# Optimization experiments

Hardware: AMD Instinct MI355X
Metric: run time of the kernel (lower is better)

The kernel has to match this reference:

```python
import jax, jax.numpy as jnp
import numpy as np

B, T, I, H, O = 1024, 512, 64, 256, 1

def setup_inputs() -> dict:
    key = jax.random.key(0)
    ks = jax.random.split(key, 12)
    s_ih0 = 1.0 / np.sqrt(H)
    def u(k, shape):
        return jax.random.uniform(k, shape, jnp.float32, -s_ih0, s_ih0)
    return {
        "x": jax.random.normal(ks[0], (B, T, I), jnp.float32),
        "w_ih0": u(ks[1], (4 * H, I)),
        "w_hh0": u(ks[2], (4 * H, H)),
        "b_ih0": u(ks[3], (4 * H,)),
        "b_hh0": u(ks[4], (4 * H,)),
        "w_ih1": u(ks[5], (4 * H, H)),
        "w_hh1": u(ks[6], (4 * H, H)),
        "b_ih1": u(ks[7], (4 * H,)),
        "b_hh1": u(ks[8], (4 * H,)),
        "fc_w": u(ks[9], (O, H)),
        "fc_b": u(ks[10], (O,)),
    }

def _lstm_layer(x, w_ih, w_hh, b_ih, b_hh):
    # x: [B, T, D_in] -> hidden sequence [B, T, H], gate order i,f,g,o (PyTorch)
    b, t, _ = x.shape
    h_dim = w_hh.shape[1]
    # precompute input projections for all timesteps: [T, B, 4H]
    xproj = (jnp.einsum('bti,gi->btg', x, w_ih) + b_ih + b_hh).transpose(1, 0, 2)
    h0 = jnp.zeros((b, h_dim), x.dtype)
    c0 = jnp.zeros((b, h_dim), x.dtype)

    def step(carry, xp):
        h, c = carry
        gates = xp + h @ w_hh.T  # [B, 4H]
        i_g, f_g, g_g, o_g = jnp.split(gates, 4, axis=-1)
        i_g = jax.nn.sigmoid(i_g)
        f_g = jax.nn.sigmoid(f_g)
        g_g = jnp.tanh(g_g)
        o_g = jax.nn.sigmoid(o_g)
        c = f_g * c + i_g * g_g
        h = o_g * jnp.tanh(c)
        return (h, c), h

    (h_last, _), hs = jax.lax.scan(step, (h0, c0), xproj)
    return hs.transpose(1, 0, 2), h_last

def reference(x, w_ih0, w_hh0, b_ih0, b_hh0, w_ih1, w_hh1, b_ih1, b_hh1, fc_w, fc_b):
    # Layer 0 -> (eval mode: dropout is identity) -> Layer 1 -> fc on last step
    h_seq0, _ = _lstm_layer(x, w_ih0, w_hh0, b_ih0, b_hh0)
    _, h_last1 = _lstm_layer(h_seq0, w_ih1, w_hh1, b_ih1, b_hh1)
    return h_last1 @ fc_w.T + fc_b  # [B, O]
```

## Files before the change

kernel.cpp:

```cpp
#include <hip/hip_runtime.h>
#include <stdint.h>


#define T_STEPS 512
#define NC0 10
#define NC1 16
#define WSLICE_ELEMS (4*(NC0+NC1)*512)
#define L1_OFF (4*NC0*512)
#define HN (1024*256)

typedef __attribute__((ext_vector_type(8))) short short8;
typedef __attribute__((ext_vector_type(4))) float floatx4;

__device__ __forceinline__ uint32_t f2bf(float f){
  uint32_t u = __builtin_bit_cast(uint32_t, f);
  return (u + 0x7fffu + ((u >> 16) & 1u)) >> 16;
}
__device__ __forceinline__ float bf2f(uint32_t b){
  return __builtin_bit_cast(float, b << 16);
}
__device__ __forceinline__ float sigm(float x){
  return __builtin_amdgcn_rcpf(1.0f + __builtin_amdgcn_exp2f(-1.44269504f*x));
}
__device__ __forceinline__ float tanhf_(float x){
  return 1.0f - 2.0f*__builtin_amdgcn_rcpf(1.0f + __builtin_amdgcn_exp2f(2.88539008f*x));
}
__device__ __forceinline__ floatx4 splat4(float v){ return (floatx4){v,v,v,v}; }

__device__ __forceinline__ short8 load_coh16(const uint16_t* p){
  short8 r;
  asm volatile("global_load_dwordx4 %0, %1, off sc0 sc1" : "=v"(r) : "v"(p));
  return r;
}
__device__ __forceinline__ void store_coh2(uint16_t* p, uint32_t v){
  asm volatile("global_store_short %0, %1, off sc0 sc1" :: "v"(p), "v"(v) : "memory");
}
__device__ __forceinline__ void vm_drain(){
  asm volatile("s_waitcnt vmcnt(0)" ::: "memory");
  __builtin_amdgcn_sched_barrier(0);
}

__device__ __forceinline__ void group_barrier(int* c, int target){
  vm_drain();
  __syncthreads();
  if (threadIdx.x == 0){
    __hip_atomic_fetch_add(c, 1, __ATOMIC_RELAXED, __HIP_MEMORY_SCOPE_AGENT);
    int spins = 0;
    while (__hip_atomic_load(c, __ATOMIC_RELAXED, __HIP_MEMORY_SCOPE_AGENT) < target){
      if (++spins > (1<<24)) break;
      __builtin_amdgcn_s_sleep(1);
    }
  }
  __syncthreads();
}

extern "C" __global__ void prep_weights(const float* __restrict__ wih0, const float* __restrict__ whh0,
                                        const float* __restrict__ wih1, const float* __restrict__ whh1,
                                        uint16_t* __restrict__ wfrag)
{
  int idx = blockIdx.x*256 + threadIdx.x;
  int s  = idx / WSLICE_ELEMS;
  int r  = idx - s*WSLICE_ELEMS;
  int layer = (r >= L1_OFF) ? 1 : 0;
  int rr = layer ? (r - L1_OFF) : r;
  int nc = layer ? NC1 : NC0;
  int n  = rr / (nc*512);
  int c  = (rr / 512) % nc;
  int l  = (rr >> 3) & 63;
  int j  = rr & 7;
  int k  = c*32 + ((l >> 4) << 3) + j;
  int grow = n*256 + s*16 + (l & 15);
  float v;
  if (!layer) v = (k < 64)  ? wih0[grow*64  + k] : whh0[grow*256 + (k - 64)];
  else        v = (k < 256) ? wih1[grow*256 + k] : whh1[grow*256 + (k - 256)];
  wfrag[idx] = (uint16_t)f2bf(v);
}

extern "C" __global__ void prep_bias(const float* __restrict__ bih0, const float* __restrict__ bhh0,
                                     const float* __restrict__ bih1, const float* __restrict__ bhh1,
                                     float* __restrict__ biasg)
{
  int idx = blockIdx.x*256 + threadIdx.x;
  if (idx >= 16*2*64) return;
  int s = idx >> 7;
  int layer = (idx >> 6) & 1;
  int q = idx & 63;
  int grow = (q >> 4)*256 + s*16 + (q & 15);
  biasg[idx] = layer ? (bih1[grow] + bhh1[grow]) : (bih0[grow] + bhh0[grow]);
}

extern "C" __global__ void __launch_bounds__(256, 1)
lstm_main(const float* __restrict__ x,
          const uint16_t* __restrict__ wfrag,
          const float* __restrict__ biasg,
          uint16_t* __restrict__ hbase,
          const float* __restrict__ fcw,
          const float* __restrict__ fcb,
          int* __restrict__ ctr,
          float* __restrict__ out)
{
  extern __shared__ uint16_t wlds[];
  const int tid  = threadIdx.x;
  const int bid  = blockIdx.x;
  const int s    = bid >> 4;
  const int g    = bid & 15;
  const int wv   = tid >> 6;
  const int lane = tid & 63;

  {
    const uint16_t* wsrc = wfrag + (size_t)s*WSLICE_ELEMS;
    for (int i = tid*8; i < WSLICE_ELEMS; i += 256*8)
      *(short8*)(wlds + i) = *(const short8*)(wsrc + i);
  }
  float b0[4], b1[4];
  {
    const int col = lane & 15;
    #pragma unroll
    for (int n = 0; n < 4; ++n){
      b0[n] = biasg[(s*2+0)*64 + n*16 + col];
      b1[n] = biasg[(s*2+1)*64 + n*16 + col];
    }
  }
  __syncthreads();

  const int arow = g*64 + wv*16 + (lane & 15);
  const int ka   = (lane >> 4) * 8;
  const int drow = g*64 + wv*16 + ((lane >> 4) << 2);
  const int dcol = s*16 + (lane & 15);

  uint16_t* h0hi[2] = { hbase + 0*(size_t)HN, hbase + 1*(size_t)HN };
  uint16_t* h0lo[2] = { hbase + 2*(size_t)HN, hbase + 3*(size_t)HN };
  uint16_t* h1hi[2] = { hbase + 4*(size_t)HN, hbase + 5*(size_t)HN };
  uint16_t* h1lo[2] = { hbase + 6*(size_t)HN, hbase + 7*(size_t)HN };

  float c0[4] = {0,0,0,0}, c1[4] = {0,0,0,0};
  int* myc = ctr + g*32;

  short8 ahi[NC0], alo[NC0];
  short8 bh[8],  bl[8];

  for (int t = 0; t < T_STEPS; ++t){
    const int par = t & 1, rpar = par ^ 1;

    {
      const float* xp = x + ((size_t)arow*T_STEPS + t)*64 + ka;
      #pragma unroll
      for (int kc = 0; kc < 2; ++kc){
        floatx4 v0 = *(const floatx4*)(xp + kc*32);
        floatx4 v1 = *(const floatx4*)(xp + kc*32 + 4);
        #pragma unroll
        for (int j = 0; j < 8; ++j){
          float f = (j < 4) ? v0[j] : v1[j-4];
          uint32_t hb = f2bf(f);
          float fh = bf2f(hb);
          uint32_t lb = f2bf(f - fh);
          ahi[kc][j] = (short)hb; alo[kc][j] = (short)lb;
        }
      }
    }
    {
      const uint16_t* ph  = h0hi[rpar] + (size_t)arow*256 + ka;
      const uint16_t* pl  = h0lo[rpar] + (size_t)arow*256 + ka;
      const uint16_t* p1h = h1hi[rpar] + (size_t)arow*256 + ka;
      const uint16_t* p1l = h1lo[rpar] + (size_t)arow*256 + ka;
      #pragma unroll
      for (int kc = 0; kc < 8; ++kc){
        ahi[2+kc] = load_coh16(ph  + kc*32);
        alo[2+kc] = load_coh16(pl  + kc*32);
        bh[kc]    = load_coh16(p1h + kc*32);
        bl[kc]    = load_coh16(p1l + kc*32);
      }
    }

    floatx4 acc[4];
    #pragma unroll
    for (int n = 0; n < 4; ++n) acc[n] = splat4(b0[n]);
    #pragma unroll
    for (int pk = 0; pk < 2; ++pk){
      #pragma unroll
      for (int n = 0; n < 4; ++n){
        short8 bfr = *(const short8*)(wlds + (n*NC0 + pk)*512 + lane*8);
        acc[n] = __builtin_amdgcn_mfma_f32_16x16x32_bf16(ahi[pk], bfr, acc[n], 0, 0, 0);
        acc[n] = __builtin_amdgcn_mfma_f32_16x16x32_bf16(alo[pk], bfr, acc[n], 0, 0, 0);
      }
    }
    vm_drain();
    #pragma unroll
    for (int pk = 2; pk < NC0; ++pk){
      #pragma unroll
      for (int n = 0; n < 4; ++n){
        short8 bfr = *(const short8*)(wlds + (n*NC0 + pk)*512 + lane*8);
        acc[n] = __builtin_amdgcn_mfma_f32_16x16x32_bf16(ahi[pk], bfr, acc[n], 0, 0, 0);
        acc[n] = __builtin_amdgcn_mfma_f32_16x16x32_bf16(alo[pk], bfr, acc[n], 0, 0, 0);
      }
    }
    {
      uint16_t* qh = h0hi[par]; uint16_t* ql = h0lo[par];
      #pragma unroll
      for (int r = 0; r < 4; ++r){
        float ig = sigm(acc[0][r]);
        float fg = sigm(acc[1][r]);
        float gg = tanhf_(acc[2][r]);
        float og = sigm(acc[3][r]);
        c0[r] = fg*c0[r] + ig*gg;
        float h = og*tanhf_(c0[r]);
        uint32_t hb = f2bf(h); float fh = bf2f(hb); uint32_t lb = f2bf(h - fh);
        size_t idx = (size_t)(drow + r)*256 + dcol;
        store_coh2(qh + idx, hb); store_coh2(ql + idx, lb);
      }
    }
    group_barrier(myc, 16*(2*t+1));

    {
      const uint16_t* p0h = h0hi[par] + (size_t)arow*256 + ka;
      const uint16_t* p0l = h0lo[par] + (size_t)arow*256 + ka;
      #pragma unroll
      for (int kc = 0; kc < 8; ++kc){
        ahi[kc] = load_coh16(p0h + kc*32);
        alo[kc] = load_coh16(p0l + kc*32);
      }
    }
    #pragma unroll
    for (int n = 0; n < 4; ++n) acc[n] = splat4(b1[n]);
    #pragma unroll
    for (int pk = 8; pk < NC1; ++pk){
      #pragma unroll
      for (int n = 0; n < 4; ++n){
        short8 bfr = *(const short8*)(wlds + L1_OFF + (n*NC1 + pk)*512 + lane*8);
        acc[n] = __builtin_amdgcn_mfma_f32_16x16x32_bf16(bh[pk-8], bfr, acc[n], 0, 0, 0);
        acc[n] = __builtin_amdgcn_mfma_f32_16x16x32_bf16(bl[pk-8], bfr, acc[n], 0, 0, 0);
      }
    }
    vm_drain();
    #pragma unroll
    for (int pk = 0; pk < 8; ++pk){
      #pragma unroll
      for (int n = 0; n < 4; ++n){
        short8 bfr = *(const short8*)(wlds + L1_OFF + (n*NC1 + pk)*512 + lane*8);
        acc[n] = __builtin_amdgcn_mfma_f32_16x16x32_bf16(ahi[pk], bfr, acc[n], 0, 0, 0);
        acc[n] = __builtin_amdgcn_mfma_f32_16x16x32_bf16(alo[pk], bfr, acc[n], 0, 0, 0);
      }
    }
    {
      uint16_t* qh = h1hi[par]; uint16_t* ql = h1lo[par];
      #pragma unroll
      for (int r = 0; r < 4; ++r){
        float ig = sigm(acc[0][r]);
        float fg = sigm(acc[1][r]);
        float gg = tanhf_(acc[2][r]);
        float og = sigm(acc[3][r]);
        c1[r] = fg*c1[r] + ig*gg;
        float h = og*tanhf_(c1[r]);
        uint32_t hb = f2bf(h); float fh = bf2f(hb); uint32_t lb = f2bf(h - fh);
        size_t idx = (size_t)(drow + r)*256 + dcol;
        store_coh2(qh + idx, hb); store_coh2(ql + idx, lb);
      }
    }
    group_barrier(myc, 16*(2*t+2));
  }

  if (s == 0){
    const uint16_t* fh = h1hi[1];
    const uint16_t* fl = h1lo[1];
    const int rl = tid >> 2, seg = tid & 3;
    const int row = g*64 + rl;
    short8 vh[8], vl[8];
    #pragma unroll
    for (int c = 0; c < 8; ++c){
      vh[c] = load_coh16(fh + (size_t)row*256 + seg*64 + c*8);
      vl[c] = load_coh16(fl + (size_t)row*256 + seg*64 + c*8);
    }
    vm_drain();
    float sum = 0.f;
    #pragma unroll
    for (int c = 0; c < 8; ++c){
      #pragma unroll
      for (int j = 0; j < 8; ++j){
        int k = seg*64 + c*8 + j;
        sum += (bf2f((uint16_t)vh[c][j]) + bf2f((uint16_t)vl[c][j])) * fcw[k];
      }
    }
    sum += __shfl_down(sum, 1);
    sum += __shfl_down(sum, 2);
    if (seg == 0) out[row] = sum + fcb[0];
  }
}

extern "C" void kernel_launch(void* const* d_in, const int* in_sizes, int n_in,
                              void* d_out, int out_size, void* d_ws, size_t ws_size,
                              hipStream_t stream)
{
  (void)in_sizes; (void)n_in; (void)out_size; (void)ws_size;
  const float* x    = (const float*)d_in[0];
  const float* wih0 = (const float*)d_in[1];
  const float* whh0 = (const float*)d_in[2];
  const float* bih0 = (const float*)d_in[3];
  const float* bhh0 = (const float*)d_in[4];
  const float* wih1 = (const float*)d_in[5];
  const float* whh1 = (const float*)d_in[6];
  const float* bih1 = (const float*)d_in[7];
  const float* bhh1 = (const float*)d_in[8];
  const float* fcw  = (const float*)d_in[9];
  const float* fcb  = (const float*)d_in[10];

  char* ws = (char*)d_ws;
  const size_t SZ_WFRAG = (size_t)16*WSLICE_ELEMS*2;
  const size_t OFF_BIAS = SZ_WFRAG;
  const size_t OFF_CTR  = OFF_BIAS + (size_t)16*2*64*4;
  const size_t OFF_H    = (size_t)2*1024*1024;

  uint16_t* wfrag = (uint16_t*)(ws);
  float*    biasg = (float*)(ws + OFF_BIAS);
  int*      ctr   = (int*)(ws + OFF_CTR);
  uint16_t* hbase = (uint16_t*)(ws + OFF_H);
  float*    out   = (float*)d_out;

  hipMemsetAsync(ws + OFF_CTR, 0, (OFF_H - OFF_CTR) + (size_t)8*HN*2, stream);

  hipLaunchKernelGGL(prep_weights, dim3(16*WSLICE_ELEMS/256), dim3(256), 0, stream,
                     wih0, whh0, wih1, whh1, wfrag);
  hipLaunchKernelGGL(prep_bias, dim3(8), dim3(256), 0, stream,
                     bih0, bhh0, bih1, bhh1, biasg);

  hipFuncSetAttribute((const void*)lstm_main,
                      hipFuncAttributeMaxDynamicSharedMemorySize, WSLICE_ELEMS*2);
  void* args[] = { (void*)&x, (void*)&wfrag, (void*)&biasg, (void*)&hbase,
                   (void*)&fcw, (void*)&fcb, (void*)&ctr, (void*)&out };
  hipLaunchCooperativeKernel((void*)lstm_main, dim3(256), dim3(256),
                             args, WSLICE_ELEMS*2, stream);
}
```

Measured before the change: 5.390 ms.

## Skew layer-1 one step behind layer-0 to halve per-step group barriers

Restructures the time loop so layer 1 processes step t-1 while layer 0 processes step t. The two layers then share one group barrier per iteration instead of two, and layer-1's input projection reuses the same loaded h0 fragments. Next-step x is prefetched and converted during compute, partial vmcnt waits replace full drains, and the final FC is fused into a last-step epilogue using shuffle reductions and atomicAdd into a zeroed output. This adds an epilogue step, a non-cooperative launch fallback, and relies on careful vmcnt counting for correctness.

```diff
diff --git a/kernel.cpp b/kernel.cpp
--- a/kernel.cpp
+++ b/kernel.cpp
@@ -27,32 +27,30 @@
 }
 __device__ __forceinline__ floatx4 splat4(float v){ return (floatx4){v,v,v,v}; }
 
+__device__ __forceinline__ void cvt8(const floatx4& v0, const floatx4& v1, short8& hi, short8& lo){
+  #pragma unroll
+  for (int j = 0; j < 8; ++j){
+    float f = (j < 4) ? v0[j] : v1[j-4];
+    uint32_t hb = f2bf(f); float fh = bf2f(hb); uint32_t lb = f2bf(f - fh);
+    hi[j] = (short)hb; lo[j] = (short)lb;
+  }
+}
+
 __device__ __forceinline__ short8 load_coh16(const uint16_t* p){
   short8 r;
   asm volatile("global_load_dwordx4 %0, %1, off sc0 sc1" : "=v"(r) : "v"(p));
   return r;
 }
+__device__ __forceinline__ floatx4 load_g16f(const float* p){
+  floatx4 r;
+  asm volatile("global_load_dwordx4 %0, %1, off" : "=v"(r) : "v"(p));
+  return r;
+}
 __device__ __forceinline__ void store_coh2(uint16_t* p, uint32_t v){
   asm volatile("global_store_short %0, %1, off sc0 sc1" :: "v"(p), "v"(v) : "memory");
 }
-__device__ __forceinline__ void vm_drain(){
-  asm volatile("s_waitcnt vmcnt(0)" ::: "memory");
-  __builtin_amdgcn_sched_barrier(0);
-}
-
-__device__ __forceinline__ void group_barrier(int* c, int target){
-  vm_drain();
-  __syncthreads();
-  if (threadIdx.x == 0){
-    __hip_atomic_fetch_add(c, 1, __ATOMIC_RELAXED, __HIP_MEMORY_SCOPE_AGENT);
-    int spins = 0;
-    while (__hip_atomic_load(c, __ATOMIC_RELAXED, __HIP_MEMORY_SCOPE_AGENT) < target){
-      if (++spins > (1<<24)) break;
-      __builtin_amdgcn_s_sleep(1);
-    }
-  }
-  __syncthreads();
-}
+#define VM_WAIT(N) do{ asm volatile("s_waitcnt vmcnt(" #N ")" ::: "memory"); \
+                       __builtin_amdgcn_sched_barrier(0); }while(0)
 
 extern "C" __global__ void prep_weights(const float* __restrict__ wih0, const float* __restrict__ whh0,
                                         const float* __restrict__ wih1, const float* __restrict__ whh1,
@@ -107,6 +105,11 @@
   const int wv   = tid >> 6;
   const int lane = tid & 63;
 
+  const int arow = g*64 + wv*16 + (lane & 15);
+  const int ka   = (lane >> 4) * 8;
+  const int drow = g*64 + wv*16 + ((lane >> 4) << 2);
+  const int dcol = s*16 + (lane & 15);
+
   {
     const uint16_t* wsrc = wfrag + (size_t)s*WSLICE_ELEMS;
     for (int i = tid*8; i < WSLICE_ELEMS; i += 256*8)
@@ -121,87 +124,93 @@
       b1[n] = biasg[(s*2+1)*64 + n*16 + col];
     }
   }
+  const float fcwv = fcw[dcol];
+  const float fcb0 = fcb[0];
+
+  short8 xh[2], xl[2];
+  {
+    const float* xp = x + (size_t)arow*T_STEPS*64 + ka;
+    floatx4 v0 = *(const floatx4*)(xp);
+    floatx4 v1 = *(const floatx4*)(xp + 4);
+    floatx4 v2 = *(const floatx4*)(xp + 32);
+    floatx4 v3 = *(const floatx4*)(xp + 36);
+    cvt8(v0, v1, xh[0], xl[0]);
+    cvt8(v2, v3, xh[1], xl[1]);
+  }
   __syncthreads();
 
-  const int arow = g*64 + wv*16 + (lane & 15);
-  const int ka   = (lane >> 4) * 8;
-  const int drow = g*64 + wv*16 + ((lane >> 4) << 2);
-  const int dcol = s*16 + (lane & 15);
-
-  uint16_t* h0hi[2] = { hbase + 0*(size_t)HN, hbase + 1*(size_t)HN };
-  uint16_t* h0lo[2] = { hbase + 2*(size_t)HN, hbase + 3*(size_t)HN };
-  uint16_t* h1hi[2] = { hbase + 4*(size_t)HN, hbase + 5*(size_t)HN };
-  uint16_t* h1lo[2] = { hbase + 6*(size_t)HN, hbase + 7*(size_t)HN };
-
+  const size_t abase = (size_t)arow*256 + ka;
   float c0[4] = {0,0,0,0}, c1[4] = {0,0,0,0};
   int* myc = ctr + g*32;
 
-  short8 ahi[NC0], alo[NC0];
-  short8 bh[8],  bl[8];
-
   for (int t = 0; t < T_STEPS; ++t){
-    const int par = t & 1, rpar = par ^ 1;
-
+    const size_t par0  = (size_t)(t & 1);
+    const size_t rpar0 = par0 ^ 1;
+
+    short8 a0h[8], a0l[8], a1h[8], a1l[8];
     {
-      const float* xp = x + ((size_t)arow*T_STEPS + t)*64 + ka;
-      #pragma unroll
-      for (int kc = 0; kc < 2; ++kc){
-        floatx4 v0 = *(const floatx4*)(xp + kc*32);
-        floatx4 v1 = *(const floatx4*)(xp + kc*32 + 4);
-        #pragma unroll
-        for (int j = 0; j < 8; ++j){
-          float f = (j < 4) ? v0[j] : v1[j-4];
-          uint32_t hb = f2bf(f);
-          float fh = bf2f(hb);
-          uint32_t lb = f2bf(f - fh);
-          ahi[kc][j] = (short)hb; alo[kc][j] = (short)lb;
-        }
-      }
+      const uint16_t* ph = hbase + rpar0*HN              + abase;
+      const uint16_t* pl = hbase + 2*(size_t)HN + rpar0*HN + abase;
+      #pragma unroll
+      for (int kc = 0; kc < 8; ++kc) a0h[kc] = load_coh16(ph + kc*32);
+      #pragma unroll
+      for (int kc = 0; kc < 8; ++kc) a0l[kc] = load_coh16(pl + kc*32);
     }
     {
-      const uint16_t* ph  = h0hi[rpar] + (size_t)arow*256 + ka;
-      const uint16_t* pl  = h0lo[rpar] + (size_t)arow*256 + ka;
-      const uint16_t* p1h = h1hi[rpar] + (size_t)arow*256 + ka;
-      const uint16_t* p1l = h1lo[rpar] + (size_t)arow*256 + ka;
-      #pragma unroll
-      for (int kc = 0; kc < 8; ++kc){
-        ahi[2+kc] = load_coh16(ph  + kc*32);
-        alo[2+kc] = load_coh16(pl  + kc*32);
-        bh[kc]    = load_coh16(p1h + kc*32);
-        bl[kc]    = load_coh16(p1l + kc*32);
-      }
-    }
-
-    floatx4 acc[4];
-    #pragma unroll
-    for (int n = 0; n < 4; ++n) acc[n] = splat4(b0[n]);
+      const uint16_t* ph = hbase + 4*(size_t)HN + par0*HN + abase;
+      const uint16_t* pl = hbase + 6*(size_t)HN + par0*HN + abase;
+      #pragma unroll
+      for (int kc = 0; kc < 8; ++kc) a1h[kc] = load_coh16(ph + kc*32);
+      #pragma unroll
+      for (int kc = 0; kc < 8; ++kc) a1l[kc] = load_coh16(pl + kc*32);
+    }
+    floatx4 xr0, xr1, xr2, xr3;
+    {
+      const int tn = (t < T_STEPS-1) ? (t+1) : t;
+      const float* xp = x + ((size_t)arow*T_STEPS + tn)*64 + ka;
+      xr0 = load_g16f(xp);      xr1 = load_g16f(xp + 4);
+      xr2 = load_g16f(xp + 32); xr3 = load_g16f(xp + 36);
+    }
+
+    floatx4 acc0[4], acc1[4];
+    #pragma unroll
+    for (int n = 0; n < 4; ++n) acc0[n] = splat4(b0[n]);
     #pragma unroll
     for (int pk = 0; pk < 2; ++pk){
       #pragma unroll
       for (int n = 0; n < 4; ++n){
-        short8 bfr = *(const short8*)(wlds + (n*NC0 + pk)*512 + lane*8);
-        acc[n] = __builtin_amdgcn_mfma_f32_16x16x32_bf16(ahi[pk], bfr, acc[n], 0, 0, 0);
-        acc[n] = __builtin_amdgcn_mfma_f32_16x16x32_bf16(alo[pk], bfr, acc[n], 0, 0, 0);
-      }
-    }
-    vm_drain();
-    #pragma unroll
-    for (int pk = 2; pk < NC0; ++pk){
+        short8 w = *(const short8*)(wlds + (n*NC0 + pk)*512 + lane*8);
+        acc0[n] = __builtin_amdgcn_mfma_f32_16x16x32_bf16(xh[pk], w, acc0[n], 0, 0, 0);
+        acc0[n] = __builtin_amdgcn_mfma_f32_16x16x32_bf16(xl[pk], w, acc0[n], 0, 0, 0);
+      }
+    }
+    #pragma unroll
+    for (int n = 0; n < 4; ++n) acc1[n] = splat4(b1[n]);
+
+    VM_WAIT(20);
+
+    #pragma unroll
+    for (int kc = 0; kc < 8; ++kc){
       #pragma unroll
       for (int n = 0; n < 4; ++n){
-        short8 bfr = *(const short8*)(wlds + (n*NC0 + pk)*512 + lane*8);
-        acc[n] = __builtin_amdgcn_mfma_f32_16x16x32_bf16(ahi[pk], bfr, acc[n], 0, 0, 0);
-        acc[n] = __builtin_amdgcn_mfma_f32_16x16x32_bf16(alo[pk], bfr, acc[n], 0, 0, 0);
-      }
-    }
+        short8 w0 = *(const short8*)(wlds + (n*NC0 + 2 + kc)*512 + lane*8);
+        acc0[n] = __builtin_amdgcn_mfma_f32_16x16x32_bf16(a0h[kc], w0, acc0[n], 0, 0, 0);
+        acc0[n] = __builtin_amdgcn_mfma_f32_16x16x32_bf16(a0l[kc], w0, acc0[n], 0, 0, 0);
+        short8 w1 = *(const short8*)(wlds + L1_OFF + (n*NC1 + kc)*512 + lane*8);
+        acc1[n] = __builtin_amdgcn_mfma_f32_16x16x32_bf16(a0h[kc], w1, acc1[n], 0, 0, 0);
+        acc1[n] = __builtin_amdgcn_mfma_f32_16x16x32_bf16(a0l[kc], w1, acc1[n], 0, 0, 0);
+      }
+    }
+
     {
-      uint16_t* qh = h0hi[par]; uint16_t* ql = h0lo[par];
+      uint16_t* qh = hbase + par0*HN;
+      uint16_t* ql = hbase + 2*(size_t)HN + par0*HN;
       #pragma unroll
       for (int r = 0; r < 4; ++r){
-        float ig = sigm(acc[0][r]);
-        float fg = sigm(acc[1][r]);
-        float gg = tanhf_(acc[2][r]);
-        float og = sigm(acc[3][r]);
+        float ig = sigm(acc0[0][r]);
+        float fg = sigm(acc0[1][r]);
+        float gg = tanhf_(acc0[2][r]);
+        float og = sigm(acc0[3][r]);
         c0[r] = fg*c0[r] + ig*gg;
         float h = og*tanhf_(c0[r]);
         uint32_t hb = f2bf(h); float fh = bf2f(hb); uint32_t lb = f2bf(h - fh);
@@ -209,46 +218,32 @@
         store_coh2(qh + idx, hb); store_coh2(ql + idx, lb);
       }
     }
-    group_barrier(myc, 16*(2*t+1));
-
-    {
-      const uint16_t* p0h = h0hi[par] + (size_t)arow*256 + ka;
-      const uint16_t* p0l = h0lo[par] + (size_t)arow*256 + ka;
-      #pragma unroll
-      for (int kc = 0; kc < 8; ++kc){
-        ahi[kc] = load_coh16(p0h + kc*32);
-        alo[kc] = load_coh16(p0l + kc*32);
-      }
-    }
-    #pragma unroll
-    for (int n = 0; n < 4; ++n) acc[n] = splat4(b1[n]);
-    #pragma unroll
-    for (int pk = 8; pk < NC1; ++pk){
+
+    VM_WAIT(12);
+
+    #pragma unroll
+    for (int kc = 0; kc < 8; ++kc){
       #pragma unroll
       for (int n = 0; n < 4; ++n){
-        short8 bfr = *(const short8*)(wlds + L1_OFF + (n*NC1 + pk)*512 + lane*8);
-        acc[n] = __builtin_amdgcn_mfma_f32_16x16x32_bf16(bh[pk-8], bfr, acc[n], 0, 0, 0);
-        acc[n] = __builtin_amdgcn_mfma_f32_16x16x32_bf16(bl[pk-8], bfr, acc[n], 0, 0, 0);
-      }
-    }
-    vm_drain();
-    #pragma unroll
-    for (int pk = 0; pk < 8; ++pk){
-      #pragma unroll
-      for (int n = 0; n < 4; ++n){
-        short8 bfr = *(const short8*)(wlds + L1_OFF + (n*NC1 + pk)*512 + lane*8);
-        acc[n] = __builtin_amdgcn_mfma_f32_16x16x32_bf16(ahi[pk], bfr, acc[n], 0, 0, 0);
-        acc[n] = __builtin_amdgcn_mfma_f32_16x16x32_bf16(alo[pk], bfr, acc[n], 0, 0, 0);
-      }
-    }
-    {
-      uint16_t* qh = h1hi[par]; uint16_t* ql = h1lo[par];
+        short8 w1 = *(const short8*)(wlds + L1_OFF + (n*NC1 + 8 + kc)*512 + lane*8);
+        acc1[n] = __builtin_amdgcn_mfma_f32_16x16x32_bf16(a1h[kc], w1, acc1[n], 0, 0, 0);
+        acc1[n] = __builtin_amdgcn_mfma_f32_16x16x32_bf16(a1l[kc], w1, acc1[n], 0, 0, 0);
+      }
+    }
+
+    VM_WAIT(8);
+    cvt8(xr0, xr1, xh[0], xl[0]);
+    cvt8(xr2, xr3, xh[1], xl[1]);
+
+    if (t > 0){
+      uint16_t* qh = hbase + 4*(size_t)HN + rpar0*HN;
+      uint16_t* ql = hbase + 6*(size_t)HN + rpar0*HN;
       #pragma unroll
       for (int r = 0; r < 4; ++r){
-        float ig = sigm(acc[0][r]);
-        float fg = sigm(acc[1][r]);
-        float gg = tanhf_(acc[2][r]);
-        float og = sigm(acc[3][r]);
+        float ig = sigm(acc1[0][r]);
+        float fg = sigm(acc1[1][r]);
+        float gg = tanhf_(acc1[2][r]);
+        float og = sigm(acc1[3][r]);
         c1[r] = fg*c1[r] + ig*gg;
         float h = og*tanhf_(c1[r]);
         uint32_t hb = f2bf(h); float fh = bf2f(hb); uint32_t lb = f2bf(h - fh);
@@ -256,33 +251,69 @@
         store_coh2(qh + idx, hb); store_coh2(ql + idx, lb);
       }
     }
-    group_barrier(myc, 16*(2*t+2));
-  }
-
-  if (s == 0){
-    const uint16_t* fh = h1hi[1];
-    const uint16_t* fl = h1lo[1];
-    const int rl = tid >> 2, seg = tid & 3;
-    const int row = g*64 + rl;
-    short8 vh[8], vl[8];
-    #pragma unroll
-    for (int c = 0; c < 8; ++c){
-      vh[c] = load_coh16(fh + (size_t)row*256 + seg*64 + c*8);
-      vl[c] = load_coh16(fl + (size_t)row*256 + seg*64 + c*8);
-    }
-    vm_drain();
-    float sum = 0.f;
-    #pragma unroll
-    for (int c = 0; c < 8; ++c){
-      #pragma unroll
-      for (int j = 0; j < 8; ++j){
-        int k = seg*64 + c*8 + j;
-        sum += (bf2f((uint16_t)vh[c][j]) + bf2f((uint16_t)vl[c][j])) * fcw[k];
-      }
-    }
-    sum += __shfl_down(sum, 1);
-    sum += __shfl_down(sum, 2);
-    if (seg == 0) out[row] = sum + fcb[0];
+
+    VM_WAIT(0);
+
+    __syncthreads();
+    if (tid == 0){
+      __hip_atomic_fetch_add(myc, 1, __ATOMIC_RELAXED, __HIP_MEMORY_SCOPE_AGENT);
+      const int target = 16*(t+1);
+      int spins = 0;
+      while (__hip_atomic_load(myc, __ATOMIC_RELAXED, __HIP_MEMORY_SCOPE_AGENT) < target){
+        if (++spins > (1<<20)) break;
+        __builtin_amdgcn_s_sleep(1);
+      }
+    }
+    __syncthreads();
+  }
+
+  {
+    const uint16_t* p0h = hbase + 1*(size_t)HN + abase;
+    const uint16_t* p0l = hbase + 3*(size_t)HN + abase;
+    const uint16_t* p1h = hbase + 4*(size_t)HN + abase;
+    const uint16_t* p1l = hbase + 6*(size_t)HN + abase;
+    short8 a0h[8], a0l[8], a1h[8], a1l[8];
+    #pragma unroll
+    for (int kc = 0; kc < 8; ++kc){
+      a0h[kc] = load_coh16(p0h + kc*32);
+      a0l[kc] = load_coh16(p0l + kc*32);
+      a1h[kc] = load_coh16(p1h + kc*32);
+      a1l[kc] = load_coh16(p1l + kc*32);
+    }
+    VM_WAIT(0);
+    floatx4 acc[4];
+    #pragma unroll
+    for (int n = 0; n < 4; ++n) acc[n] = splat4(b1[n]);
+    #pragma unroll
+    for (int kc = 0; kc < 8; ++kc){
+      #pragma unroll
+      for (int n = 0; n < 4; ++n){
+        short8 w1 = *(const short8*)(wlds + L1_OFF + (n*NC1 + kc)*512 + lane*8);
+        acc[n] = __builtin_amdgcn_mfma_f32_16x16x32_bf16(a0h[kc], w1, acc[n], 0, 0, 0);
+        acc[n] = __builtin_amdgcn_mfma_f32_16x16x32_bf16(a0l[kc], w1, acc[n], 0, 0, 0);
+        short8 w2 = *(const short8*)(wlds + L1_OFF + (n*NC1 + 8 + kc)*512 + lane*8);
+        acc[n] = __builtin_amdgcn_mfma_f32_16x16x32_bf16(a1h[kc], w2, acc[n], 0, 0, 0);
+        acc[n] = __builtin_amdgcn_mfma_f32_16x16x32_bf16(a1l[kc], w2, acc[n], 0, 0, 0);
+      }
+    }
+    #pragma unroll
+    for (int r = 0; r < 4; ++r){
+      float ig = sigm(acc[0][r]);
+      float fg = sigm(acc[1][r]);
+      float gg = tanhf_(acc[2][r]);
+      float og = sigm(acc[3][r]);
+      float cc = fg*c1[r] + ig*gg;
+      float h  = og*tanhf_(cc);
+      float v  = h * fcwv;
+      v += __shfl_xor(v, 1);
+      v += __shfl_xor(v, 2);
+      v += __shfl_xor(v, 4);
+      v += __shfl_xor(v, 8);
+      if ((lane & 15) == 0){
+        float res = v + ((s == 0) ? fcb0 : 0.0f);
+        atomicAdd(out + drow + r, res);
+      }
+    }
   }
 }
 
@@ -315,6 +346,7 @@
   uint16_t* hbase = (uint16_t*)(ws + OFF_H);
   float*    out   = (float*)d_out;
 
+  hipMemsetAsync(d_out, 0, (size_t)1024*sizeof(float), stream);
   hipMemsetAsync(ws + OFF_CTR, 0, (OFF_H - OFF_CTR) + (size_t)8*HN*2, stream);
 
   hipLaunchKernelGGL(prep_weights, dim3(16*WSLICE_ELEMS/256), dim3(256), 0, stream,
@@ -326,6 +358,10 @@
                       hipFuncAttributeMaxDynamicSharedMemorySize, WSLICE_ELEMS*2);
   void* args[] = { (void*)&x, (void*)&wfrag, (void*)&biasg, (void*)&hbase,
                    (void*)&fcw, (void*)&fcb, (void*)&ctr, (void*)&out };
-  hipLaunchCooperativeKernel((void*)lstm_main, dim3(256), dim3(256),
-                             args, WSLICE_ELEMS*2, stream);
-}
+  hipError_t ce = hipLaunchCooperativeKernel((void*)lstm_main, dim3(256), dim3(256),
+                                             args, WSLICE_ELEMS*2, stream);
+  if (ce != hipSuccess){
+    hipLaunchKernelGGL(lstm_main, dim3(256), dim3(256), WSLICE_ELEMS*2, stream,
+                       x, wfrag, biasg, hbase, fcw, fcb, ctr, out);
+  }
+}
```

Result: faster. 4.642 ms (-13.9%).
